# Kernel tuning notes

Measured on AMD Instinct MI355X. Metric: run time of the kernel, lower is better.

## Reference

```python
import jax, jax.numpy as jnp
import numpy as np
import math

B, S, H = 4, 2048, 1024
NE, NC, CD, OD = 4, 16, 64, 128  # num_experiments, num_exp_codes, exp_code_dim, outcome_dim
TAU, TEMP, EPS = 0.5, 0.07, 1e-5


def gelu(x):
    return jax.nn.gelu(x, approximate=False)


def layer_norm(x, g, b):
    m = x.mean(-1, keepdims=True)
    v = ((x - m) ** 2).mean(-1, keepdims=True)
    return (x - m) * jax.lax.rsqrt(v + EPS) * g + b


def setup_inputs() -> dict:
    key = jax.random.key(0)
    ks = jax.random.split(key, 24)
    lin = lambda k, i, o: jax.random.normal(k, (i, o), jnp.float32) * 0.02
    u = jax.random.uniform(ks[1], (B, NE, NC), minval=1e-6, maxval=1.0 - 1e-6)
    d = {
        "hidden_states": jax.random.normal(ks[0], (B, S, H), jnp.float32),
        "attention_mask": jnp.ones((B, S), jnp.int32),
        "gumbel_noise": -jnp.log(-jnp.log(u)),
        # context_pooler: Linear(H,H) + LayerNorm
        "cp_w": lin(ks[2], H, H), "cp_b": jnp.zeros(H), "cp_ln_g": jnp.ones(H), "cp_ln_b": jnp.zeros(H),
        # eph: Linear(H,H), Linear(H, NE*NC)
        "eph_w1": lin(ks[3], H, H), "eph_b1": jnp.zeros(H),
        "eph_w2": lin(ks[4], H, NE * NC), "eph_b2": jnp.zeros(NE * NC),
        "codebook": jax.random.normal(ks[5], (NC, CD), jnp.float32) * 0.02,
        # world_kernel: Linear(H+CD, 2H), Linear(2H, OD)
        "wk_w1": lin(ks[6], H + CD, 2 * H), "wk_b1": jnp.zeros(2 * H),
        "wk_w2": lin(ks[7], 2 * H, OD), "wk_b2": jnp.zeros(OD),
        "tp_w": lin(ks[8], H, OD),  # target_proj, no bias
        # film_proj: Linear(OD, 2H) + GELU
        "film_w": lin(ks[9], OD, 2 * H), "film_b": jnp.zeros(2 * H),
        "q_w": lin(ks[10], H, H), "q_b": jnp.zeros(H),
        "k_w": lin(ks[11], H, H), "k_b": jnp.zeros(H),
        "v_w": lin(ks[12], H, H), "v_b": jnp.zeros(H),
        "o_w": lin(ks[13], H, H), "o_b": jnp.zeros(H),
        "int_w": lin(ks[14], H, 4 * H), "int_b": jnp.zeros(4 * H),
        "out_w": lin(ks[15], 4 * H, H), "out_b": jnp.zeros(H),
        "ln_g": jnp.ones(H), "ln_b": jnp.zeros(H),
    }
    return d


def reference(hidden_states, attention_mask, gumbel_noise,
              cp_w, cp_b, cp_ln_g, cp_ln_b,
              eph_w1, eph_b1, eph_w2, eph_b2, codebook,
              wk_w1, wk_b1, wk_w2, wk_b2, tp_w, film_w, film_b,
              q_w, q_b, k_w, k_b, v_w, v_b, o_w, o_b,
              int_w, int_b, out_w, out_b, ln_g, ln_b):
    mask = attention_mask.astype(hidden_states.dtype)  # [B,S]
    # --- context pooling ---
    denom = mask.sum(1, keepdims=True) + 1e-8
    pooled = (hidden_states * mask[:, :, None]).sum(1) / denom  # [B,H]
    h_ctx = layer_norm(gelu(pooled @ cp_w + cp_b), cp_ln_g, cp_ln_b)
    # --- experiment proposal (gumbel-softmax, hard, tau=0.5) ---
    z_raw = gelu(h_ctx @ eph_w1 + eph_b1) @ eph_w2 + eph_b2
    z_logits = z_raw.reshape(B, NE, NC)
    y_soft = jax.nn.softmax((z_logits + gumbel_noise) / TAU, axis=-1)
    y_hard = jax.nn.one_hot(jnp.argmax(y_soft, -1), NC, dtype=y_soft.dtype)
    z_soft = y_hard - jax.lax.stop_gradient(y_soft) + y_soft  # straight-through
    z_codes = z_soft @ codebook  # [B,NE,CD]
    # --- world kernel ---
    h_rep = jnp.broadcast_to(h_ctx[:, None, :], (B, NE, H))
    h_wk = jnp.concatenate([h_rep, z_codes], -1)  # [B,NE,H+CD]
    outcome = gelu(h_wk @ wk_w1 + wk_b1) @ wk_w2 + wk_b2  # [B,NE,OD]
    # --- info gain (labels/plan_vector None branch) ---
    tv = h_ctx @ tp_w
    tv = tv / jnp.linalg.norm(tv, axis=-1, keepdims=True).clip(1e-12)
    on = outcome / jnp.linalg.norm(outcome, axis=-1, keepdims=True).clip(1e-12)
    info_gain = jnp.sum(on * tv[:, None, :], -1) / TEMP  # [B,NE]
    idx = jnp.argmax(info_gain, -1)  # [B]
    chosen = jnp.take_along_axis(outcome, idx[:, None, None], axis=1)[:, 0]  # [B,OD]
    # --- FiLM ---
    gb = gelu(chosen @ film_w + film_b)  # [B,2H]
    gamma, beta = gb[:, :H], gb[:, H:]
    fused = gamma[:, None, :] * hidden_states + beta[:, None, :]  # [B,S,H]
    # --- single-head attention ---
    q = fused @ q_w + q_b
    k = fused @ k_w + k_b
    v = fused @ v_w + v_b
    scores = jnp.einsum('bqd,bkd->bqk', q, k) / math.sqrt(H)
    scores = jnp.where(attention_mask[:, None, :] == 0, -jnp.inf, scores)
    attn = jax.nn.softmax(scores, axis=-1)
    attn_out = jnp.einsum('bqk,bkd->bqd', attn, v) @ o_w + o_b
    # --- FFN + residual + LN ---
    ff = gelu((attn_out + fused) @ int_w + int_b) @ out_w + out_b
    return layer_norm(ff + fused, ln_g, ln_b)
```

## Files before the change

### kernel.cpp

```cpp
#include <hip/hip_runtime.h>
#include <math.h>

#define DEVI __device__ __forceinline__

typedef unsigned short u16;
typedef __attribute__((ext_vector_type(4))) float f32x4;
typedef __attribute__((ext_vector_type(8))) short s16x8;
typedef __attribute__((ext_vector_type(4))) short s16x4;

constexpr int Bc = 4, Sc = 2048, Hc = 1024;
constexpr int NEc = 4, NCc = 16, CDc = 64, ODc = 128;
constexpr float TAUc = 0.5f, TEMPc = 0.07f, EPSc = 1e-5f;

DEVI float gelu_f(float x) { return 0.5f * x * (1.0f + erff(x * 0.7071067811865476f)); }

DEVI float bf2f(u16 u) { union { unsigned int i; float f; } v; v.i = ((unsigned int)u) << 16; return v.f; }
DEVI u16 f2bf(float f) {
  union { float f; unsigned int i; } v; v.f = f;
  unsigned int u = v.i;
  unsigned int r = (u + 0x7fffu + ((u >> 16) & 1u)) >> 16;
  return (u16)r;
}

DEVI float wred_sum(float v) {
  #pragma unroll
  for (int o = 32; o > 0; o >>= 1) v += __shfl_down(v, o);
  return v;
}
DEVI float wred_max(float v) {
  #pragma unroll
  for (int o = 32; o > 0; o >>= 1) v = fmaxf(v, __shfl_down(v, o));
  return v;
}

DEVI void gload16(const void* g, void* l) {
  __builtin_amdgcn_global_load_lds((const __attribute__((address_space(1))) void*)g,
                                   (__attribute__((address_space(3))) void*)l, 16, 0, 0);
}

template<int EPI>
__global__ __launch_bounds__(256, 3) void gemm_bt(
    const u16* __restrict__ A, long sAz, int lda,
    const u16* __restrict__ Bt, long sBz, int ldb,
    u16* __restrict__ C, long sCz, int ldc,
    const float* __restrict__ bias,
    const u16* __restrict__ resid, long sRz,
    float scale, int M, int N, int K)
{
  const int bz = blockIdx.z;
  A += (long)bz * sAz; Bt += (long)bz * sBz; C += (long)bz * sCz;
  if (EPI & 4) resid += (long)bz * sRz;

  int bid = blockIdx.x;
  const int nwg = gridDim.x;
  if ((nwg & 7) == 0) bid = ((bid & 7) * (nwg >> 3)) + (bid >> 3);

  const int nTn = N >> 7;
  const int tm = bid / nTn, tn = bid % nTn;
  const int tid = threadIdx.x;
  const int wid = tid >> 6, lane = tid & 63;
  const int wr = wid >> 1, wc = wid & 1;
  const int l15 = lane & 15, l4 = lane >> 4;

  __shared__ u16 smem[9216];
  u16* As = smem;
  u16* Bs = smem + 4096;

  f32x4 acc[4][4];
  #pragma unroll
  for (int i = 0; i < 4; ++i)
    #pragma unroll
    for (int j = 0; j < 4; ++j) acc[i][j] = f32x4{0.f, 0.f, 0.f, 0.f};

  const int srow = (wid << 5) + (lane >> 2);
  const int scol = (lane & 3) << 3;
  const u16* aS = A + (long)(tm * 128 + srow) * lda + scol;
  const u16* bS = Bt + (long)(tn * 128 + srow) * ldb + scol;
  const long aStep16 = (long)16 * lda;
  const long bStep16 = (long)16 * ldb;
  u16* aD = &As[wid * 32 * 32];
  u16* bD = &Bs[wid * 32 * 32];

  for (int k0 = 0; k0 < K; k0 += 32) {
    gload16(aS, aD);
    gload16(aS + aStep16, aD + 16 * 32);
    gload16(bS, bD);
    gload16(bS + bStep16, bD + 16 * 32);
    __syncthreads();
    s16x8 af[4], bfr[4];
    #pragma unroll
    for (int i = 0; i < 4; ++i) {
      const int row = (wr << 6) + (i << 4) + l15;
      af[i] = *(const s16x8*)&As[(row << 5) + (l4 << 3)];
    }
    #pragma unroll
    for (int j = 0; j < 4; ++j) {
      const int col = (wc << 6) + (j << 4) + l15;
      bfr[j] = *(const s16x8*)&Bs[(col << 5) + (l4 << 3)];
    }
    #pragma unroll
    for (int i = 0; i < 4; ++i)
      #pragma unroll
      for (int j = 0; j < 4; ++j)
        acc[i][j] = __builtin_amdgcn_mfma_f32_16x16x32_bf16(af[i], bfr[j], acc[i][j], 0, 0, 0);
    __syncthreads();
    aS += 32; bS += 32;
  }

  if (!(EPI & 8)) {
    u16 (*Cs)[128] = (u16(*)[128])smem;
    #pragma unroll
    for (int p = 0; p < 2; ++p) {
      if (wr == p) {
        #pragma unroll
        for (int j = 0; j < 4; ++j) {
          const int c = (wc << 6) + (j << 4) + l15;
          const float bv = (EPI & 1) ? bias[tn * 128 + c] : 0.f;
          #pragma unroll
          for (int i = 0; i < 4; ++i) {
            const int lr = (i << 4) + (l4 << 2);
            #pragma unroll
            for (int r = 0; r < 4; ++r) {
              float v = acc[i][j][r] * scale + bv;
              if (EPI & 2) v = gelu_f(v);
              Cs[lr + r][c] = f2bf(v);
            }
          }
        }
      }
      __syncthreads();
      #pragma unroll
      for (int it = 0; it < 4; ++it) {
        const int row = (tid >> 4) + (it << 4);
        const int chunk = tid & 15;
        const long Gr = tm * 128 + (p << 6) + row;
        const int col0 = tn * 128 + (chunk << 3);
        s16x8 cv = *(s16x8*)&Cs[row][chunk << 3];
        if (EPI & 4) {
          const s16x8 rv = *(const s16x8*)&resid[Gr * ldc + col0];
          #pragma unroll
          for (int e = 0; e < 8; ++e)
            cv[e] = (short)f2bf(bf2f((u16)cv[e]) + bf2f((u16)rv[e]));
        }
        *(s16x8*)&C[Gr * ldc + col0] = cv;
      }
      if (p == 0) __syncthreads();
    }
  } else {
    u16 (*Ct)[136] = (u16(*)[136])smem;
    #pragma unroll
    for (int p = 0; p < 2; ++p) {
      if (wc == p) {
        #pragma unroll
        for (int j = 0; j < 4; ++j) {
          const int lc = (j << 4) + l15;
          const float bv = (EPI & 1) ? bias[tn * 128 + (p << 6) + lc] : 0.f;
          #pragma unroll
          for (int i = 0; i < 4; ++i) {
            const int row_lo = (wr << 6) + (i << 4) + (l4 << 2);
            s16x4 pk;
            #pragma unroll
            for (int r = 0; r < 4; ++r) {
              float v = acc[i][j][r] * scale + bv;
              if (EPI & 2) v = gelu_f(v);
              pk[r] = (short)f2bf(v);
            }
            *(s16x4*)&Ct[lc][row_lo] = pk;
          }
        }
      }
      __syncthreads();
      #pragma unroll
      for (int it = 0; it < 4; ++it) {
        const int lc = (tid >> 4) + (it << 4);
        const int chunk = tid & 15;
        const long Gc = tn * 128 + (p << 6) + lc;
        const int col0 = tm * 128 + (chunk << 3);
        s16x8 cv = *(s16x8*)&Ct[lc][chunk << 3];
        *(s16x8*)&C[Gc * ldc + col0] = cv;
      }
      if (p == 0) __syncthreads();
    }
  }
}

__global__ void transpose_w_k(const float* __restrict__ in, u16* __restrict__ out, int K, int N) {
  __shared__ float t[32][33];
  const int n0 = blockIdx.x << 5, k0 = blockIdx.y << 5;
  const int tx = threadIdx.x, ty = threadIdx.y;
  #pragma unroll
  for (int i = 0; i < 32; i += 8)
    t[ty + i][tx] = in[(long)(k0 + ty + i) * N + n0 + tx];
  __syncthreads();
  #pragma unroll
  for (int i = 0; i < 32; i += 8)
    out[(long)(n0 + ty + i) * K + k0 + tx] = f2bf(t[tx][ty + i]);
}

__global__ void transpose_w4_k(const float* __restrict__ w0, const float* __restrict__ w1,
                               const float* __restrict__ w2, const float* __restrict__ w3,
                               u16* __restrict__ o0, u16* __restrict__ o1,
                               u16* __restrict__ o2, u16* __restrict__ o3) {
  const int z = blockIdx.z;
  const float* in = (z == 0) ? w0 : (z == 1) ? w1 : (z == 2) ? w2 : w3;
  u16* out = (z == 0) ? o0 : (z == 1) ? o1 : (z == 2) ? o2 : o3;
  __shared__ float t[32][33];
  const int n0 = blockIdx.x << 5, k0 = blockIdx.y << 5;
  const int tx = threadIdx.x, ty = threadIdx.y;
  #pragma unroll
  for (int i = 0; i < 32; i += 8)
    t[ty + i][tx] = in[(long)(k0 + ty + i) * Hc + n0 + tx];
  __syncthreads();
  #pragma unroll
  for (int i = 0; i < 32; i += 8)
    out[(long)(n0 + ty + i) * Hc + k0 + tx] = f2bf(t[tx][ty + i]);
}

__global__ void concat_bias_k(const float* __restrict__ a, const float* __restrict__ b,
                              float* __restrict__ o) {
  const int i = (blockIdx.x << 8) + threadIdx.x;
  o[i] = (i < Hc) ? a[i] : b[i - Hc];
}

__global__ void pool_partial_k(const float* __restrict__ hs, const int* __restrict__ mask,
                               float* __restrict__ part) {
  const int h = (blockIdx.x << 8) + threadIdx.x;
  const int c = blockIdx.y, b = blockIdx.z;
  const int s0 = c * (Sc / 16);
  float acc = 0.f;
  for (int i = 0; i < Sc / 16; ++i) {
    const int s = s0 + i;
    acc += hs[((long)b * Sc + s) * Hc + h] * (float)mask[b * Sc + s];
  }
  part[((b << 4) + c) * Hc + h] = acc;
}

__global__ void pool_final_k(const float* __restrict__ part, const int* __restrict__ mask,
                             float* __restrict__ pooled) {
  const int b = blockIdx.x;
  __shared__ float red[4];
  __shared__ float denom_s;
  float d = 0.f;
  for (int i = threadIdx.x; i < Sc; i += 256) d += (float)mask[b * Sc + i];
  d = wred_sum(d);
  if ((threadIdx.x & 63) == 0) red[threadIdx.x >> 6] = d;
  __syncthreads();
  if (threadIdx.x == 0) denom_s = red[0] + red[1] + red[2] + red[3] + 1e-8f;
  __syncthreads();
  const float inv = 1.f / denom_s;
  for (int h = threadIdx.x; h < Hc; h += 256) {
    float s = 0.f;
    #pragma unroll
    for (int c = 0; c < 16; ++c) s += part[((b << 4) + c) * Hc + h];
    pooled[b * Hc + h] = s * inv;
  }
}

template<int R>
__global__ void mrow_part_k(const float* __restrict__ in, const float* __restrict__ W,
                            float* __restrict__ part, int K, int N) {
  const int t = threadIdx.x;
  const int jj = t & 31;
  const int j = (blockIdx.x << 5) + jj;
  const int ks = t >> 5;
  const int nchunk = gridDim.y;
  const int Kc = K / (nchunk << 3);
  const int k0 = ((blockIdx.y << 3) + ks) * Kc;
  float acc[R];
  #pragma unroll
  for (int r = 0; r < R; ++r) acc[r] = 0.f;
  for (int k = k0; k < k0 + Kc; ++k) {
    const float wv = W[(long)k * N + j];
    #pragma unroll
    for (int r = 0; r < R; ++r) acc[r] = fmaf(in[r * K + k], wv, acc[r]);
  }
  __shared__ float sm[8][R][32];
  #pragma unroll
  for (int r = 0; r < R; ++r) sm[ks][r][jj] = acc[r];
  __syncthreads();
  for (int idx = t; idx < R * 32; idx += 256) {
    const int r = idx >> 5, j2 = idx & 31;
    float s = 0.f;
    #pragma unroll
    for (int q = 0; q < 8; ++q) s += sm[q][r][j2];
    part[(long)(blockIdx.y * R + r) * N + (blockIdx.x << 5) + j2] = s;
  }
}

template<bool GELU>
__global__ void mrow_reduce_k(const float* __restrict__ part, const float* __restrict__ bias,
                              float* __restrict__ out, int N, int R, int nchunk) {
  const int idx = (blockIdx.x << 8) + threadIdx.x;
  if (idx >= R * N) return;
  const int r = idx / N, j = idx - r * N;
  float s = 0.f;
  for (int c = 0; c < nchunk; ++c) s += part[(long)(c * R + r) * N + j];
  if (bias) s += bias[j];
  if (GELU) s = gelu_f(s);
  out[(long)r * N + j] = s;
}

__global__ void ln_rows_k(float* __restrict__ x, const float* __restrict__ g,
                          const float* __restrict__ b) {
  const long base = (long)blockIdx.x * Hc;
  __shared__ float red[4];
  float v[4]; float s = 0.f;
  #pragma unroll
  for (int i = 0; i < 4; ++i) { v[i] = x[base + threadIdx.x + (i << 8)]; s += v[i]; }
  s = wred_sum(s);
  if ((threadIdx.x & 63) == 0) red[threadIdx.x >> 6] = s;
  __syncthreads();
  const float mean = (red[0] + red[1] + red[2] + red[3]) * (1.f / Hc);
  float q = 0.f;
  #pragma unroll
  for (int i = 0; i < 4; ++i) { const float d2 = v[i] - mean; q += d2 * d2; }
  __syncthreads();
  q = wred_sum(q);
  if ((threadIdx.x & 63) == 0) red[threadIdx.x >> 6] = q;
  __syncthreads();
  const float var = (red[0] + red[1] + red[2] + red[3]) * (1.f / Hc);
  const float inv = rsqrtf(var + EPSc);
  #pragma unroll
  for (int i = 0; i < 4; ++i) {
    const int col = threadIdx.x + (i << 8);
    x[base + col] = (v[i] - mean) * inv * g[col] + b[col];
  }
}

__global__ void gumbel_k(const float* __restrict__ z, const float* __restrict__ gn,
                         const float* __restrict__ cb, float* __restrict__ zcodes) {
  const int b = blockIdx.x, t = threadIdx.x;
  if (t >= NEc) return;
  const float* zp = z + b * (NEc * NCc) + t * NCc;
  const float* gp = gn + (b * NEc + t) * NCc;
  int best = 0; float bv = -3.4e38f;
  for (int c2 = 0; c2 < NCc; ++c2) {
    const float val = (zp[c2] + gp[c2]) * (1.f / TAUc);
    if (val > bv) { bv = val; best = c2; }
  }
  for (int d2 = 0; d2 < CDc; ++d2)
    zcodes[(b * NEc + t) * CDc + d2] = cb[best * CDc + d2];
}

__global__ void build_hwk_k(const float* __restrict__ hctx, const float* __restrict__ zcodes,
                            float* __restrict__ hwk) {
  const int r = blockIdx.x;
  const int b = r >> 2;
  for (int i = threadIdx.x; i < Hc + CDc; i += 256)
    hwk[r * (Hc + CDc) + i] = (i < Hc) ? hctx[b * Hc + i] : zcodes[r * CDc + (i - Hc)];
}

__global__ void select_k(const float* __restrict__ tv, const float* __restrict__ outc,
                         float* __restrict__ chosen) {
  const int b = blockIdx.x, t = threadIdx.x;
  __shared__ float red[2];
  __shared__ float ig[NEc];
  __shared__ int bestIdx;
  const float x = tv[b * ODc + t];
  float ss = wred_sum(x * x);
  if ((t & 63) == 0) red[t >> 6] = ss;
  __syncthreads();
  float nrm = fmaxf(sqrtf(red[0] + red[1]), 1e-12f);
  const float tvn = x / nrm;
  __syncthreads();
  for (int ne = 0; ne < NEc; ++ne) {
    const float o = outc[(b * NEc + ne) * ODc + t];
    float a = wred_sum(o * o);
    float d2 = wred_sum(o * tvn);
    if ((t & 63) == 0) red[t >> 6] = a;
    __syncthreads();
    const float no = sqrtf(red[0] + red[1]);
    __syncthreads();
    if ((t & 63) == 0) red[t >> 6] = d2;
    __syncthreads();
    const float dd = red[0] + red[1];
    if (t == 0) ig[ne] = dd / fmaxf(no, 1e-12f) * (1.f / TEMPc);
    __syncthreads();
  }
  if (t == 0) {
    int bi = 0; float bvv = ig[0];
    for (int ne = 1; ne < NEc; ++ne) if (ig[ne] > bvv) { bvv = ig[ne]; bi = ne; }
    bestIdx = bi;
  }
  __syncthreads();
  chosen[b * ODc + t] = outc[(b * NEc + bestIdx) * ODc + t];
}

__global__ void fuse_k(const float* __restrict__ hs, const float* __restrict__ gb,
                       u16* __restrict__ fused) {
  const long i = (((long)blockIdx.x << 8) + threadIdx.x) << 2;
  const int h = (int)(i & (Hc - 1));
  const int b = (int)(i >> 21);
  const float4 xv = *(const float4*)(hs + i);
  const float* gp = gb + b * 2048;
  s16x4 pk = { (short)f2bf(fmaf(gp[h + 0], xv.x, gp[Hc + h + 0])),
               (short)f2bf(fmaf(gp[h + 1], xv.y, gp[Hc + h + 1])),
               (short)f2bf(fmaf(gp[h + 2], xv.z, gp[Hc + h + 2])),
               (short)f2bf(fmaf(gp[h + 3], xv.w, gp[Hc + h + 3])) };
  *(s16x4*)(fused + i) = pk;
}

__global__ void softmax_k(u16* __restrict__ sc, const int* __restrict__ mask) {
  const long base = (long)blockIdx.x * Sc;
  const int b = blockIdx.x / Sc;
  __shared__ float red[4];
  float x[8];
  float mx = -3.0e38f;
  #pragma unroll
  for (int i = 0; i < 8; ++i) {
    const int col = threadIdx.x + (i << 8);
    float v = bf2f(sc[base + col]);
    if (mask[b * Sc + col] == 0) v = -3.0e38f;
    x[i] = v;
    mx = fmaxf(mx, v);
  }
  mx = wred_max(mx);
  if ((threadIdx.x & 63) == 0) red[threadIdx.x >> 6] = mx;
  __syncthreads();
  mx = fmaxf(fmaxf(red[0], red[1]), fmaxf(red[2], red[3]));
  float sum = 0.f;
  #pragma unroll
  for (int i = 0; i < 8; ++i) { x[i] = __expf(x[i] - mx); sum += x[i]; }
  __syncthreads();
  sum = wred_sum(sum);
  if ((threadIdx.x & 63) == 0) red[threadIdx.x >> 6] = sum;
  __syncthreads();
  const float inv = 1.f / (red[0] + red[1] + red[2] + red[3]);
  #pragma unroll
  for (int i = 0; i < 8; ++i)
    sc[base + threadIdx.x + (i << 8)] = f2bf(x[i] * inv);
}

__global__ void final_ln_k(const u16* __restrict__ ff, const u16* __restrict__ fused,
                           const float* __restrict__ g, const float* __restrict__ b,
                           float* __restrict__ out) {
  const long base = (long)blockIdx.x * Hc;
  __shared__ float red[4];
  float v[4]; float s = 0.f;
  #pragma unroll
  for (int i = 0; i < 4; ++i) {
    const int col = threadIdx.x + (i << 8);
    v[i] = bf2f(ff[base + col]) + bf2f(fused[base + col]);
    s += v[i];
  }
  s = wred_sum(s);
  if ((threadIdx.x & 63) == 0) red[threadIdx.x >> 6] = s;
  __syncthreads();
  const float mean = (red[0] + red[1] + red[2] + red[3]) * (1.f / Hc);
  float q = 0.f;
  #pragma unroll
  for (int i = 0; i < 4; ++i) { const float d2 = v[i] - mean; q += d2 * d2; }
  __syncthreads();
  q = wred_sum(q);
  if ((threadIdx.x & 63) == 0) red[threadIdx.x >> 6] = q;
  __syncthreads();
  const float var = (red[0] + red[1] + red[2] + red[3]) * (1.f / Hc);
  const float inv = rsqrtf(var + EPSc);
  #pragma unroll
  for (int i = 0; i < 4; ++i) {
    const int col = threadIdx.x + (i << 8);
    out[base + col] = (v[i] - mean) * inv * g[col] + b[col];
  }
}

extern "C" void kernel_launch(void* const* d_in, const int* in_sizes, int n_in,
                              void* d_out, int out_size, void* d_ws, size_t ws_size,
                              hipStream_t stream) {
  const float* hs       = (const float*)d_in[0];
  const int*   amask    = (const int*)d_in[1];
  const float* gn       = (const float*)d_in[2];
  const float* cp_w     = (const float*)d_in[3];
  const float* cp_b     = (const float*)d_in[4];
  const float* cp_ln_g  = (const float*)d_in[5];
  const float* cp_ln_b  = (const float*)d_in[6];
  const float* eph_w1   = (const float*)d_in[7];
  const float* eph_b1   = (const float*)d_in[8];
  const float* eph_w2   = (const float*)d_in[9];
  const float* eph_b2   = (const float*)d_in[10];
  const float* codebook = (const float*)d_in[11];
  const float* wk_w1    = (const float*)d_in[12];
  const float* wk_b1    = (const float*)d_in[13];
  const float* wk_w2    = (const float*)d_in[14];
  const float* wk_b2    = (const float*)d_in[15];
  const float* tp_w     = (const float*)d_in[16];
  const float* film_w   = (const float*)d_in[17];
  const float* film_b   = (const float*)d_in[18];
  const float* q_w      = (const float*)d_in[19];
  const float* q_bias   = (const float*)d_in[20];
  const float* k_w      = (const float*)d_in[21];
  const float* k_bias   = (const float*)d_in[22];
  const float* v_w      = (const float*)d_in[23];
  const float* v_bias   = (const float*)d_in[24];
  const float* o_w      = (const float*)d_in[25];
  const float* o_bias   = (const float*)d_in[26];
  const float* int_w    = (const float*)d_in[27];
  const float* int_b    = (const float*)d_in[28];
  const float* out_w    = (const float*)d_in[29];
  const float* out_b    = (const float*)d_in[30];
  const float* ln_g     = (const float*)d_in[31];
  const float* ln_b     = (const float*)d_in[32];
  float* outp = (float*)d_out;

  char* w = (char*)d_ws;
  auto alloc = [&](size_t bytes) -> char* {
    char* p = w; w += (bytes + 255) & ~(size_t)255; return p;
  };
  float* part    = (float*)alloc((size_t)Bc * 16 * Hc * 4);
  float* pooled  = (float*)alloc((size_t)Bc * Hc * 4);
  float* hctx    = (float*)alloc((size_t)Bc * Hc * 4);
  float* t1      = (float*)alloc((size_t)Bc * Hc * 4);
  float* zlog    = (float*)alloc((size_t)Bc * 64 * 4);
  float* zcodes  = (float*)alloc((size_t)Bc * NEc * CDc * 4);
  float* hwk     = (float*)alloc((size_t)16 * (Hc + CDc) * 4);
  float* wkt1    = (float*)alloc((size_t)16 * 2048 * 4);
  float* outcome = (float*)alloc((size_t)16 * ODc * 4);
  float* tvb     = (float*)alloc((size_t)Bc * ODc * 4);
  float* chosen  = (float*)alloc((size_t)Bc * ODc * 4);
  float* gb      = (float*)alloc((size_t)Bc * 2048 * 4);
  float* lin_part= (float*)alloc((size_t)1024 * 1024);
  float* qk_bias = (float*)alloc((size_t)2048 * 4);
  u16* qT    = (u16*)alloc((size_t)Hc * Hc * 2);
  u16* kT    = (u16*)alloc((size_t)Hc * Hc * 2);
  u16* vTw   = (u16*)alloc((size_t)Hc * Hc * 2);
  u16* oT    = (u16*)alloc((size_t)Hc * Hc * 2);
  u16* intT  = (u16*)alloc((size_t)Hc * 4096 * 2);
  u16* outT  = (u16*)alloc((size_t)Hc * 4096 * 2);
  u16* fused = (u16*)alloc((size_t)8192 * Hc * 2);
  u16* qkact = (u16*)alloc((size_t)8192 * 2048 * 2);
  u16* scores= (u16*)alloc((size_t)Bc * Sc * Sc * 2);
  u16* vTact = (u16*)alloc((size_t)8192 * Hc * 2);
  u16* attn  = (u16*)alloc((size_t)8192 * Hc * 2);
  u16* h1    = (u16*)alloc((size_t)8192 * Hc * 2);
  u16* mid = qkact;
  u16* ffo = attn;

  if ((size_t)(w - (char*)d_ws) > ws_size) return;

  const dim3 tb32(32, 8);
  transpose_w4_k<<<dim3(32, 32, 4), tb32, 0, stream>>>(q_w, k_w, v_w, o_w, qT, kT, vTw, oT);
  transpose_w_k<<<dim3(4096 / 32, Hc / 32), tb32, 0, stream>>>(int_w, intT, Hc, 4096);
  transpose_w_k<<<dim3(Hc / 32, 4096 / 32), tb32, 0, stream>>>(out_w, outT, 4096, Hc);
  concat_bias_k<<<8, 256, 0, stream>>>(q_bias, k_bias, qk_bias);

  pool_partial_k<<<dim3(Hc / 256, 16, Bc), 256, 0, stream>>>(hs, amask, part);
  pool_final_k<<<Bc, 256, 0, stream>>>(part, amask, pooled);

  mrow_part_k<4><<<dim3(32, 8), 256, 0, stream>>>(pooled, cp_w, lin_part, Hc, Hc);
  mrow_reduce_k<true><<<16, 256, 0, stream>>>(lin_part, cp_b, hctx, Hc, 4, 8);
  ln_rows_k<<<Bc, 256, 0, stream>>>(hctx, cp_ln_g, cp_ln_b);
  mrow_part_k<4><<<dim3(32, 8), 256, 0, stream>>>(hctx, eph_w1, lin_part, Hc, Hc);
  mrow_reduce_k<true><<<16, 256, 0, stream>>>(lin_part, eph_b1, t1, Hc, 4, 8);
  mrow_part_k<4><<<dim3(2, 16), 256, 0, stream>>>(t1, eph_w2, lin_part, Hc, 64);
  mrow_reduce_k<false><<<1, 256, 0, stream>>>(lin_part, eph_b2, zlog, 64, 4, 16);
  gumbel_k<<<Bc, 64, 0, stream>>>(zlog, gn, codebook, zcodes);
  build_hwk_k<<<Bc * NEc, 256, 0, stream>>>(hctx, zcodes, hwk);
  mrow_part_k<16><<<dim3(64, 8), 256, 0, stream>>>(hwk, wk_w1, lin_part, Hc + CDc, 2048);
  mrow_reduce_k<true><<<128, 256, 0, stream>>>(lin_part, wk_b1, wkt1, 2048, 16, 8);
  mrow_part_k<16><<<dim3(4, 32), 256, 0, stream>>>(wkt1, wk_w2, lin_part, 2048, ODc);
  mrow_reduce_k<false><<<8, 256, 0, stream>>>(lin_part, wk_b2, outcome, ODc, 16, 32);
  mrow_part_k<4><<<dim3(4, 8), 256, 0, stream>>>(hctx, tp_w, lin_part, Hc, ODc);
  mrow_reduce_k<false><<<2, 256, 0, stream>>>(lin_part, nullptr, tvb, ODc, 4, 8);
  select_k<<<Bc, 128, 0, stream>>>(tvb, outcome, chosen);
  mrow_part_k<4><<<dim3(64, 2), 256, 0, stream>>>(chosen, film_w, lin_part, ODc, 2048);
  mrow_reduce_k<true><<<32, 256, 0, stream>>>(lin_part, film_b, gb, 2048, 4, 2);
  fuse_k<<<8192, 256, 0, stream>>>(hs, gb, fused);

  gemm_bt<1><<<dim3(1024), 256, 0, stream>>>(fused, 0, Hc, qT, 0, Hc, qkact, 0, 2048,
                                             qk_bias, nullptr, 0, 1.f, 8192, 2048, Hc);
  gemm_bt<9><<<dim3(512), 256, 0, stream>>>(fused, 0, Hc, vTw, 0, Hc, vTact, 0, 8192,
                                            v_bias, nullptr, 0, 1.f, 8192, Hc, Hc);
  gemm_bt<0><<<dim3(256, 1, Bc), 256, 0, stream>>>(qkact, (long)Sc * 2048, 2048,
                                                   qkact + 1024, (long)Sc * 2048, 2048,
                                                   scores, (long)Sc * Sc, Sc,
                                                   nullptr, nullptr, 0, 0.03125f, Sc, Sc, Hc);
  softmax_k<<<Bc * Sc, 256, 0, stream>>>(scores, amask);
  gemm_bt<0><<<dim3(128, 1, Bc), 256, 0, stream>>>(scores, (long)Sc * Sc, Sc,
                                                   vTact, (long)Sc, 8192,
                                                   attn, (long)Sc * Hc, Hc,
                                                   nullptr, nullptr, 0, 1.f, Sc, Hc, Sc);
  gemm_bt<5><<<dim3(512), 256, 0, stream>>>(attn, 0, Hc, oT, 0, Hc, h1, 0, Hc,
                                            o_bias, fused, 0, 1.f, 8192, Hc, Hc);
  gemm_bt<3><<<dim3(2048), 256, 0, stream>>>(h1, 0, Hc, intT, 0, Hc, mid, 0, 4096,
                                             int_b, nullptr, 0, 1.f, 8192, 4096, Hc);
  gemm_bt<1><<<dim3(512), 256, 0, stream>>>(mid, 0, 4096, outT, 0, 4096, ffo, 0, Hc,
                                            out_b, nullptr, 0, 1.f, 8192, Hc, 4096);
  final_ln_k<<<Bc * Sc, 256, 0, stream>>>(ffo, fused, ln_g, ln_b, outp);
}
```

Baseline: 560.2 us.

## Add 256x256 eight-wave pipelined GEMM and route most projections through it

Adds a new GEMM kernel with 256x256 output tiles, 512 threads (8 waves) and a double-buffered 128 KB LDS pool. Loads for the next K-step are interleaved between the four MFMA sub-phases, with explicit waitcnts, barriers and priority raises during compute. The epilogue stages output through LDS for coalesced stores and fuses bias, GELU and residual. All large GEMMs except the V projection now use it, aiming for more data reuse per tile and better overlap of load and compute. The trade-off is fewer blocks: the o-proj and out-proj grids have only 128 tiles, which can leave compute units idle, and the large LDS footprint allows about one block per CU.

```diff
diff --git a/kernel.cpp b/kernel.cpp
--- a/kernel.cpp
+++ b/kernel.cpp
@@ -36,6 +36,193 @@
 DEVI void gload16(const void* g, void* l) {
   __builtin_amdgcn_global_load_lds((const __attribute__((address_space(1))) void*)g,
                                    (__attribute__((address_space(3))) void*)l, 16, 0, 0);
+}
+
+template<int EPI>
+__global__ __launch_bounds__(512, 2) void gemm8(
+    const u16* __restrict__ A, long sAz, int lda,
+    const u16* __restrict__ Bt, long sBz, int ldb,
+    u16* __restrict__ C, long sCz, int ldc,
+    const float* __restrict__ bias,
+    const u16* __restrict__ resid, long sRz,
+    float scale, int N, int K)
+{
+  const int bz = blockIdx.z;
+  A += (long)bz * sAz; Bt += (long)bz * sBz; C += (long)bz * sCz;
+  const u16* Rp = (EPI & 4) ? (resid + (long)bz * sRz) : nullptr;
+
+  int bid = blockIdx.x;
+  const int nwg = gridDim.x;
+  bid = ((bid & 7) * (nwg >> 3)) + (bid >> 3);
+  const int nTn = N >> 8;
+  const int tm = bid / nTn, tn = bid - tm * nTn;
+
+  const int tid = threadIdx.x;
+  const int lane = tid & 63;
+  const int wid = tid >> 6;
+  const int wm = wid >> 2, wn = wid & 3;
+  const int l15 = lane & 15, l4 = lane >> 4;
+
+  __shared__ u16 pool[65536];
+
+  const int nkt = K >> 6;
+  const int srow = tid >> 3, schunk = tid & 7;
+
+  const u16* Ab = A + (long)(tm * 256) * lda;
+  const u16* Bb = Bt + (long)(tn * 256) * ldb;
+
+  auto stA = [&](int b, int h, int kt) {
+    #pragma unroll
+    for (int L = 0; L < 2; ++L) {
+      const int lr = h * 128 + srow + L * 64;
+      gload16(Ab + (long)lr * lda + (kt << 6) + ((schunk ^ (lr & 7)) << 3),
+              &pool[b * 16384 + lr * 64 + schunk * 8]);
+    }
+  };
+  auto stB = [&](int b, int h, int kt) {
+    #pragma unroll
+    for (int L = 0; L < 2; ++L) {
+      const int lr = h * 128 + srow + L * 64;
+      gload16(Bb + (long)lr * ldb + (kt << 6) + ((schunk ^ (lr & 7)) << 3),
+              &pool[32768 + b * 16384 + lr * 64 + schunk * 8]);
+    }
+  };
+
+  f32x4 acc[8][4];
+  #pragma unroll
+  for (int m = 0; m < 8; ++m)
+    #pragma unroll
+    for (int n = 0; n < 4; ++n) acc[m][n] = f32x4{0.f, 0.f, 0.f, 0.f};
+
+  const int aBase = (wm * 128 + l15) * 64;
+  const int bBase = 32768 + (wn * 64 + l15) * 64;
+  const int cx0 = ((l4 ^ (l15 & 7)) << 3);
+  const int cx1 = (((4 + l4) ^ (l15 & 7)) << 3);
+
+  s16x8 af[4], bf[2][4];
+
+  stA(0, 0, 0); stA(0, 1, 0); stB(0, 0, 0); stB(0, 1, 0);
+  if (nkt > 1) {
+    stB(1, 0, 1); stB(1, 1, 1); stA(1, 0, 1);
+    asm volatile("s_waitcnt vmcnt(6)" ::: "memory");
+  } else {
+    asm volatile("s_waitcnt vmcnt(0)" ::: "memory");
+  }
+  __builtin_amdgcn_s_barrier();
+
+  for (int kt = 0; kt < nkt; ++kt) {
+    const int b = kt & 1, bb16 = b * 16384;
+    #pragma unroll
+    for (int m = 0; m < 4; ++m) af[m] = *(const s16x8*)&pool[bb16 + aBase + m * 1024 + cx0];
+    #pragma unroll
+    for (int n = 0; n < 4; ++n) bf[0][n] = *(const s16x8*)&pool[bb16 + bBase + n * 1024 + cx0];
+    __builtin_amdgcn_sched_barrier(0);
+    __builtin_amdgcn_s_barrier();
+    asm volatile("s_waitcnt lgkmcnt(0)" ::: "memory");
+    __builtin_amdgcn_sched_barrier(0);
+    if (kt + 1 < nkt) stA(b ^ 1, 1, kt + 1);
+    __builtin_amdgcn_s_setprio(1);
+    #pragma unroll
+    for (int m = 0; m < 4; ++m)
+      #pragma unroll
+      for (int n = 0; n < 4; ++n)
+        acc[m][n] = __builtin_amdgcn_mfma_f32_16x16x32_bf16(af[m], bf[0][n], acc[m][n], 0, 0, 0);
+    __builtin_amdgcn_s_setprio(0);
+    __builtin_amdgcn_sched_barrier(0);
+    __builtin_amdgcn_s_barrier();
+    #pragma unroll
+    for (int m = 0; m < 4; ++m) af[m] = *(const s16x8*)&pool[bb16 + aBase + m * 1024 + cx1];
+    #pragma unroll
+    for (int n = 0; n < 4; ++n) bf[1][n] = *(const s16x8*)&pool[bb16 + bBase + n * 1024 + cx1];
+    __builtin_amdgcn_sched_barrier(0);
+    __builtin_amdgcn_s_barrier();
+    asm volatile("s_waitcnt lgkmcnt(0)" ::: "memory");
+    __builtin_amdgcn_sched_barrier(0);
+    if (kt + 2 < nkt) stB(b, 0, kt + 2);
+    __builtin_amdgcn_s_setprio(1);
+    #pragma unroll
+    for (int m = 0; m < 4; ++m)
+      #pragma unroll
+      for (int n = 0; n < 4; ++n)
+        acc[m][n] = __builtin_amdgcn_mfma_f32_16x16x32_bf16(af[m], bf[1][n], acc[m][n], 0, 0, 0);
+    __builtin_amdgcn_s_setprio(0);
+    __builtin_amdgcn_sched_barrier(0);
+    __builtin_amdgcn_s_barrier();
+    #pragma unroll
+    for (int m = 0; m < 4; ++m) af[m] = *(const s16x8*)&pool[bb16 + aBase + (m + 4) * 1024 + cx0];
+    __builtin_amdgcn_sched_barrier(0);
+    __builtin_amdgcn_s_barrier();
+    asm volatile("s_waitcnt lgkmcnt(0)" ::: "memory");
+    __builtin_amdgcn_sched_barrier(0);
+    if (kt + 2 < nkt) stB(b, 1, kt + 2);
+    __builtin_amdgcn_s_setprio(1);
+    #pragma unroll
+    for (int m = 0; m < 4; ++m)
+      #pragma unroll
+      for (int n = 0; n < 4; ++n)
+        acc[m + 4][n] = __builtin_amdgcn_mfma_f32_16x16x32_bf16(af[m], bf[0][n], acc[m + 4][n], 0, 0, 0);
+    __builtin_amdgcn_s_setprio(0);
+    __builtin_amdgcn_sched_barrier(0);
+    __builtin_amdgcn_s_barrier();
+    #pragma unroll
+    for (int m = 0; m < 4; ++m) af[m] = *(const s16x8*)&pool[bb16 + aBase + (m + 4) * 1024 + cx1];
+    __builtin_amdgcn_sched_barrier(0);
+    __builtin_amdgcn_s_barrier();
+    asm volatile("s_waitcnt lgkmcnt(0)" ::: "memory");
+    __builtin_amdgcn_sched_barrier(0);
+    if (kt + 2 < nkt) stA(b, 0, kt + 2);
+    __builtin_amdgcn_s_setprio(1);
+    #pragma unroll
+    for (int m = 0; m < 4; ++m)
+      #pragma unroll
+      for (int n = 0; n < 4; ++n)
+        acc[m + 4][n] = __builtin_amdgcn_mfma_f32_16x16x32_bf16(af[m], bf[1][n], acc[m + 4][n], 0, 0, 0);
+    __builtin_amdgcn_s_setprio(0);
+    if (kt < nkt - 2) asm volatile("s_waitcnt vmcnt(6)" ::: "memory");
+    else              asm volatile("s_waitcnt vmcnt(0)" ::: "memory");
+    __builtin_amdgcn_sched_barrier(0);
+    __builtin_amdgcn_s_barrier();
+  }
+
+  float bvn[4];
+  #pragma unroll
+  for (int n = 0; n < 4; ++n)
+    bvn[n] = (EPI & 1) ? bias[tn * 256 + wn * 64 + n * 16 + l15] : 0.f;
+
+  for (int p = 0; p < 2; ++p) {
+    if (wm == p) {
+      #pragma unroll
+      for (int m = 0; m < 8; ++m)
+        #pragma unroll
+        for (int n = 0; n < 4; ++n) {
+          const int lc = wn * 64 + n * 16 + l15;
+          #pragma unroll
+          for (int r = 0; r < 4; ++r) {
+            float v = acc[m][n][r] * scale + bvn[n];
+            if (EPI & 2) v = gelu_f(v);
+            pool[(m * 16 + l4 * 4 + r) * 264 + lc] = f2bf(v);
+          }
+        }
+    }
+    __syncthreads();
+    const long gr0 = (long)tm * 256 + p * 128;
+    #pragma unroll
+    for (int it = 0; it < 8; ++it) {
+      const int row = (tid >> 5) + it * 16;
+      const int ch = tid & 31;
+      const long Gr = gr0 + row;
+      const int col0 = tn * 256 + ch * 8;
+      s16x8 cv = *(s16x8*)&pool[row * 264 + ch * 8];
+      if (EPI & 4) {
+        const s16x8 rv = *(const s16x8*)&Rp[Gr * ldc + col0];
+        #pragma unroll
+        for (int e = 0; e < 8; ++e)
+          cv[e] = (short)f2bf(bf2f((u16)cv[e]) + bf2f((u16)rv[e]));
+      }
+      *(s16x8*)&C[Gr * ldc + col0] = cv;
+    }
+    __syncthreads();
+  }
 }
 
 template<int EPI>
@@ -565,24 +752,24 @@
   mrow_reduce_k<true><<<32, 256, 0, stream>>>(lin_part, film_b, gb, 2048, 4, 2);
   fuse_k<<<8192, 256, 0, stream>>>(hs, gb, fused);
 
-  gemm_bt<1><<<dim3(1024), 256, 0, stream>>>(fused, 0, Hc, qT, 0, Hc, qkact, 0, 2048,
-                                             qk_bias, nullptr, 0, 1.f, 8192, 2048, Hc);
+  gemm8<1><<<dim3(256), 512, 0, stream>>>(fused, 0, Hc, qT, 0, Hc, qkact, 0, 2048,
+                                          qk_bias, nullptr, 0, 1.f, 2048, Hc);
   gemm_bt<9><<<dim3(512), 256, 0, stream>>>(fused, 0, Hc, vTw, 0, Hc, vTact, 0, 8192,
                                             v_bias, nullptr, 0, 1.f, 8192, Hc, Hc);
-  gemm_bt<0><<<dim3(256, 1, Bc), 256, 0, stream>>>(qkact, (long)Sc * 2048, 2048,
-                                                   qkact + 1024, (long)Sc * 2048, 2048,
-                                                   scores, (long)Sc * Sc, Sc,
-                                                   nullptr, nullptr, 0, 0.03125f, Sc, Sc, Hc);
+  gemm8<0><<<dim3(64, 1, Bc), 512, 0, stream>>>(qkact, (long)Sc * 2048, 2048,
+                                                qkact + 1024, (long)Sc * 2048, 2048,
+                                                scores, (long)Sc * Sc, Sc,
+                                                nullptr, nullptr, 0, 0.03125f, Sc, Hc);
   softmax_k<<<Bc * Sc, 256, 0, stream>>>(scores, amask);
-  gemm_bt<0><<<dim3(128, 1, Bc), 256, 0, stream>>>(scores, (long)Sc * Sc, Sc,
-                                                   vTact, (long)Sc, 8192,
-                                                   attn, (long)Sc * Hc, Hc,
-                                                   nullptr, nullptr, 0, 1.f, Sc, Hc, Sc);
-  gemm_bt<5><<<dim3(512), 256, 0, stream>>>(attn, 0, Hc, oT, 0, Hc, h1, 0, Hc,
-                                            o_bias, fused, 0, 1.f, 8192, Hc, Hc);
-  gemm_bt<3><<<dim3(2048), 256, 0, stream>>>(h1, 0, Hc, intT, 0, Hc, mid, 0, 4096,
-                                             int_b, nullptr, 0, 1.f, 8192, 4096, Hc);
-  gemm_bt<1><<<dim3(512), 256, 0, stream>>>(mid, 0, 4096, outT, 0, 4096, ffo, 0, Hc,
-                                            out_b, nullptr, 0, 1.f, 8192, Hc, 4096);
+  gemm8<0><<<dim3(32, 1, Bc), 512, 0, stream>>>(scores, (long)Sc * Sc, Sc,
+                                                vTact, 2048, 8192,
+                                                attn, (long)Sc * Hc, Hc,
+                                                nullptr, nullptr, 0, 1.f, Hc, Sc);
+  gemm8<5><<<dim3(128), 512, 0, stream>>>(attn, 0, Hc, oT, 0, Hc, h1, 0, Hc,
+                                          o_bias, fused, 0, 1.f, Hc, Hc);
+  gemm8<3><<<dim3(512), 512, 0, stream>>>(h1, 0, Hc, intT, 0, Hc, mid, 0, 4096,
+                                          int_b, nullptr, 0, 1.f, 4096, Hc);
+  gemm8<1><<<dim3(128), 512, 0, stream>>>(mid, 0, 4096, outT, 0, 4096, ffo, 0, Hc,
+                                          out_b, nullptr, 0, 1.f, Hc, 4096);
   final_ln_k<<<Bc * Sc, 256, 0, stream>>>(ffo, fused, ln_g, ln_b, outp);
 }
```

Result: slower. 916.4 us (+63.6%).

## Double GEMM K-tile to 64 with XOR-swizzled LDS and vectorize softmax I/O

Applied to the files above, without the earlier changes.

The GEMM main loop now stages a 64-wide K slice per iteration instead of 32. It uses an XOR-swizzled LDS layout so the 16-byte fragment reads avoid bank conflicts, and each synchronization pair now covers twice as many MFMAs. The softmax kernel switches from strided scalar bf16 loads and stores to 16-byte vector loads and stores per thread, with vectorized mask reads. LDS use per block grows from about 18KB to 32KB, which may lower occupancy.

```diff
diff --git a/kernel.cpp b/kernel.cpp
--- a/kernel.cpp
+++ b/kernel.cpp
@@ -62,9 +62,9 @@
   const int wr = wid >> 1, wc = wid & 1;
   const int l15 = lane & 15, l4 = lane >> 4;
 
-  __shared__ u16 smem[9216];
+  __shared__ u16 smem[16384];
   u16* As = smem;
-  u16* Bs = smem + 4096;
+  u16* Bs = smem + 8192;
 
   f32x4 acc[4][4];
   #pragma unroll
@@ -72,39 +72,42 @@
     #pragma unroll
     for (int j = 0; j < 4; ++j) acc[i][j] = f32x4{0.f, 0.f, 0.f, 0.f};
 
-  const int srow = (wid << 5) + (lane >> 2);
-  const int scol = (lane & 3) << 3;
-  const u16* aS = A + (long)(tm * 128 + srow) * lda + scol;
-  const u16* bS = Bt + (long)(tn * 128 + srow) * ldb + scol;
-  const long aStep16 = (long)16 * lda;
-  const long bStep16 = (long)16 * ldb;
-  u16* aD = &As[wid * 32 * 32];
-  u16* bD = &Bs[wid * 32 * 32];
-
-  for (int k0 = 0; k0 < K; k0 += 32) {
-    gload16(aS, aD);
-    gload16(aS + aStep16, aD + 16 * 32);
-    gload16(bS, bD);
-    gload16(bS + bStep16, bD + 16 * 32);
+  const int srow8 = lane >> 3;
+  const int scol = (((lane & 7) ^ srow8) << 3);
+  const u16* aS = A + (long)(tm * 128 + (wid << 5) + srow8) * lda + scol;
+  const u16* bS = Bt + (long)(tn * 128 + (wid << 5) + srow8) * ldb + scol;
+  u16* aD = &As[wid * 2048];
+  u16* bD = &Bs[wid * 2048];
+
+  const int x7 = l15 & 7;
+  const int cx0 = ((l4 ^ x7) << 3);
+  const int cx1 = (((l4 + 4) ^ x7) << 3);
+
+  for (int k0 = 0; k0 < K; k0 += 64) {
+    #pragma unroll
+    for (int L = 0; L < 4; ++L) {
+      gload16(aS + (long)(L * 8) * lda, aD + L * 512);
+      gload16(bS + (long)(L * 8) * ldb, bD + L * 512);
+    }
     __syncthreads();
-    s16x8 af[4], bfr[4];
-    #pragma unroll
-    for (int i = 0; i < 4; ++i) {
-      const int row = (wr << 6) + (i << 4) + l15;
-      af[i] = *(const s16x8*)&As[(row << 5) + (l4 << 3)];
-    }
-    #pragma unroll
-    for (int j = 0; j < 4; ++j) {
-      const int col = (wc << 6) + (j << 4) + l15;
-      bfr[j] = *(const s16x8*)&Bs[(col << 5) + (l4 << 3)];
-    }
-    #pragma unroll
-    for (int i = 0; i < 4; ++i)
+    #pragma unroll
+    for (int ks = 0; ks < 2; ++ks) {
+      const int cx = ks ? cx1 : cx0;
+      s16x8 af[4], bfr[4];
+      #pragma unroll
+      for (int i = 0; i < 4; ++i)
+        af[i] = *(const s16x8*)&As[((wr << 6) + (i << 4) + l15) * 64 + cx];
       #pragma unroll
       for (int j = 0; j < 4; ++j)
-        acc[i][j] = __builtin_amdgcn_mfma_f32_16x16x32_bf16(af[i], bfr[j], acc[i][j], 0, 0, 0);
+        bfr[j] = *(const s16x8*)&Bs[((wc << 6) + (j << 4) + l15) * 64 + cx];
+      #pragma unroll
+      for (int i = 0; i < 4; ++i)
+        #pragma unroll
+        for (int j = 0; j < 4; ++j)
+          acc[i][j] = __builtin_amdgcn_mfma_f32_16x16x32_bf16(af[i], bfr[j], acc[i][j], 0, 0, 0);
+    }
     __syncthreads();
-    aS += 32; bS += 32;
+    aS += 64; bS += 64;
   }
 
   if (!(EPI & 8)) {
@@ -403,19 +406,25 @@
 __global__ void softmax_k(u16* __restrict__ sc, const int* __restrict__ mask) {
   const long base = (long)blockIdx.x * Sc;
   const int b = blockIdx.x / Sc;
+  const int t = threadIdx.x;
   __shared__ float red[4];
+  s16x8 v8 = *(s16x8*)&sc[base + t * 8];
+  const int4 m0 = *(const int4*)&mask[b * Sc + t * 8];
+  const int4 m1 = *(const int4*)&mask[b * Sc + t * 8 + 4];
   float x[8];
+  x[0] = (m0.x == 0) ? -3.0e38f : bf2f((u16)v8[0]);
+  x[1] = (m0.y == 0) ? -3.0e38f : bf2f((u16)v8[1]);
+  x[2] = (m0.z == 0) ? -3.0e38f : bf2f((u16)v8[2]);
+  x[3] = (m0.w == 0) ? -3.0e38f : bf2f((u16)v8[3]);
+  x[4] = (m1.x == 0) ? -3.0e38f : bf2f((u16)v8[4]);
+  x[5] = (m1.y == 0) ? -3.0e38f : bf2f((u16)v8[5]);
+  x[6] = (m1.z == 0) ? -3.0e38f : bf2f((u16)v8[6]);
+  x[7] = (m1.w == 0) ? -3.0e38f : bf2f((u16)v8[7]);
   float mx = -3.0e38f;
   #pragma unroll
-  for (int i = 0; i < 8; ++i) {
-    const int col = threadIdx.x + (i << 8);
-    float v = bf2f(sc[base + col]);
-    if (mask[b * Sc + col] == 0) v = -3.0e38f;
-    x[i] = v;
-    mx = fmaxf(mx, v);
-  }
+  for (int i = 0; i < 8; ++i) mx = fmaxf(mx, x[i]);
   mx = wred_max(mx);
-  if ((threadIdx.x & 63) == 0) red[threadIdx.x >> 6] = mx;
+  if ((t & 63) == 0) red[t >> 6] = mx;
   __syncthreads();
   mx = fmaxf(fmaxf(red[0], red[1]), fmaxf(red[2], red[3]));
   float sum = 0.f;
@@ -423,12 +432,13 @@
   for (int i = 0; i < 8; ++i) { x[i] = __expf(x[i] - mx); sum += x[i]; }
   __syncthreads();
   sum = wred_sum(sum);
-  if ((threadIdx.x & 63) == 0) red[threadIdx.x >> 6] = sum;
+  if ((t & 63) == 0) red[t >> 6] = sum;
   __syncthreads();
   const float inv = 1.f / (red[0] + red[1] + red[2] + red[3]);
-  #pragma unroll
-  for (int i = 0; i < 8; ++i)
-    sc[base + threadIdx.x + (i << 8)] = f2bf(x[i] * inv);
+  s16x8 o8;
+  #pragma unroll
+  for (int i = 0; i < 8; ++i) o8[i] = (short)f2bf(x[i] * inv);
+  *(s16x8*)&sc[base + t * 8] = o8;
 }
 
 __global__ void final_ln_k(const u16* __restrict__ ff, const u16* __restrict__ fused,
```

After: 492.3 us. 12.1% less time.
